# Kernel tuning notes

Hardware: AMD Instinct MI355X
Metric: run time of the kernel (lower is better)

Reference implementation:

```python
import jax, jax.numpy as jnp
import numpy as np

B, N, E = 64, 128, 512
F_NODE, F_EDGE = 16, 8
NODE_SIZE = EDGE_SIZE = 64
NUM_STEPS, N_ITER, OMEGA = 3, 8, 0.75
CUTOFF, SMEAR, EPS = 50.0, -0.39, 1e-6


def mila(x):
    # mila with beta=-1: x * tanh(softplus(x - 1))
    return x * jnp.tanh(jax.nn.softplus(x - 1.0))


def ssp(x):
    return jax.nn.softplus(x) + 1e-3


def setup_inputs():
    key = jax.random.key(0)
    ks = iter(jax.random.split(key, 64))
    def nrm(shape, s=1.0):
        return jax.random.normal(next(ks), shape, jnp.float32) * s
    def he(shape):
        return nrm(shape, (2.0 / shape[-2]) ** 0.5)
    inp = {}
    inp['nodes1'] = nrm((N, F_NODE))
    inp['edges1'] = nrm((E, F_EDGE))
    inp['senders1'] = jax.random.randint(next(ks), (E,), 0, N)
    inp['receivers1'] = jax.random.randint(next(ks), (E,), 0, N)
    inp['nodes2'] = nrm((N, F_NODE))
    inp['edges2'] = nrm((E, F_EDGE))
    inp['senders2'] = jax.random.randint(next(ks), (E,), 0, N)
    inp['receivers2'] = jax.random.randint(next(ks), (E,), 0, N)
    c1 = jax.random.uniform(next(ks), (B, N, 3), jnp.float32, 0.0, 10.0)
    c2 = jax.random.uniform(next(ks), (B, N, 3), jnp.float32, 0.0, 10.0) + jnp.array([12.0, 0.0, 0.0])
    inp['coords1'], inp['coords2'] = c1, c2
    inp['distance_matrices'] = jnp.linalg.norm(c1[:, :, None, :] - c2[:, None, :, :], axis=-1)
    inp['multipoles'] = nrm((2, B, N, 1), 0.2)
    inp['W_emb_node'], inp['b_emb_node'] = he((F_NODE, NODE_SIZE)), jnp.zeros((NODE_SIZE,))
    inp['W_emb_edge'], inp['b_emb_edge'] = he((F_EDGE, EDGE_SIZE)), jnp.zeros((EDGE_SIZE,))
    inp['W_gn_edge'] = he((NUM_STEPS, EDGE_SIZE + 2 * NODE_SIZE, EDGE_SIZE))
    inp['b_gn_edge'] = jnp.zeros((NUM_STEPS, EDGE_SIZE))
    inp['W_gn_node'] = he((NUM_STEPS, NODE_SIZE + EDGE_SIZE, NODE_SIZE))
    inp['b_gn_node'] = jnp.zeros((NUM_STEPS, NODE_SIZE))
    inp['pp_W0'], inp['pp_b0'] = he((2 * NODE_SIZE, NODE_SIZE)), jnp.zeros((NODE_SIZE,))
    inp['pp_W1'], inp['pp_b1'] = he((NODE_SIZE, NODE_SIZE)), jnp.zeros((NODE_SIZE,))
    inp['pp_W2'], inp['pp_b2'] = he((NODE_SIZE, 5)), jnp.zeros((5,))
    inp['ap_W0'], inp['ap_b0'] = he((NODE_SIZE, NODE_SIZE)), jnp.zeros((NODE_SIZE,))
    inp['ap_W1'], inp['ap_b1'] = he((NODE_SIZE, NODE_SIZE)), jnp.zeros((NODE_SIZE,))
    inp['ap_W2'], inp['ap_b2'] = he((NODE_SIZE, 5)), jnp.zeros((5,))
    return inp


def _gnn(nodes, edges, senders, receivers, Wen, ben, Wee, bee, Wge, bge, Wgn, bgn):
    # GraphIndependent embedding, then NUM_STEPS InteractionNetwork blocks
    n = mila(nodes @ Wen + ben)
    e = mila(edges @ Wee + bee)
    for s in range(NUM_STEPS):
        e_in = jnp.concatenate([e, n[receivers], n[senders]], axis=-1)
        e = mila(e_in @ Wge[s] + bge[s])
        agg = jax.ops.segment_sum(e, receivers, num_segments=N)
        n = mila(jnp.concatenate([n, agg], axis=-1) @ Wgn[s] + bgn[s])
    return n


def _mlp3(x, W0, b0, W1, b1, W2, b2):
    h = mila(x @ W0 + b0)
    h = mila(h @ W1 + b1)
    return ssp(h @ W2 + b2)


def _induction(coords1, coords2, pol1, pol2, dist, q1, q2):
    # Thole-damped SCF induced dipoles between the two monomers
    r12 = coords1[:, :, None, :] - coords2[:, None, :, :]            # [B,N,N,3]
    R = dist[..., None]                                              # [B,N,N,1]
    R3 = R ** 3 + EPS
    au = jnp.sqrt(pol1[:, 0][:, None] * pol2[:, 0][None, :]) + EPS   # [N,N]
    u3 = dist ** 3 / au                                              # [B,N,N]
    exu = jnp.exp(SMEAR * u3)
    lam3 = (1.0 - exu)[..., None]
    lam5 = (1.0 - (1.0 - SMEAR * u3) * exu)[..., None]
    E0_1 = jnp.sum(q2[:, None, :, None] * lam3 * r12 / R3, axis=2)   # [B,N,3]
    E0_2 = jnp.sum(q1[:, :, None, None] * lam3 * (-r12) / R3, axis=1)
    eye = jnp.eye(3, dtype=coords1.dtype)
    T12 = (3.0 * lam5[..., None] * r12[..., :, None] * r12[..., None, :] / (R ** 5 + EPS)[..., None]
           - lam3[..., None] * eye / R3[..., None])                  # [B,N,N,3,3]
    p1, p2 = pol1[None], pol2[None]                                  # [1,N,1]
    mu1, mu2 = p1 * E0_1, p2 * E0_2
    def step(carry, _):
        m1, m2 = carry
        f1 = E0_1 + jnp.einsum('bijkl,bjl->bik', T12, m2)
        f2 = E0_2 + jnp.einsum('bijkl,bil->bjk', T12, m1)
        m1n = (1.0 - OMEGA) * m1 + OMEGA * p1 * f1
        m2n = (1.0 - OMEGA) * m2 + OMEGA * p2 * f2
        return (m1n, m2n), None
    (mu1, mu2), _ = jax.lax.scan(step, (mu1, mu2), None, length=N_ITER)
    energy = -0.5 * (jnp.sum(mu1 * E0_1, axis=(1, 2)) + jnp.sum(mu2 * E0_2, axis=(1, 2)))
    return energy, mu1, mu2


def _forward(nodes1, edges1, senders1, receivers1, nodes2, edges2, senders2, receivers2,
             coords1, coords2, multipoles, distance_matrices,
             W_emb_node, b_emb_node, W_emb_edge, b_emb_edge,
             W_gn_edge, b_gn_edge, W_gn_node, b_gn_node,
             pp_W0, pp_b0, pp_W1, pp_b1, pp_W2, pp_b2,
             ap_W0, ap_b0, ap_W1, ap_b1, ap_W2, ap_b2):
    Bsz = distance_matrices.shape[0]
    h1 = jnp.argmax(nodes1, axis=-1) == 0
    h2 = jnp.argmax(nodes2, axis=-1) == 0
    i1 = jnp.repeat(jnp.arange(N), N)
    i2 = jnp.tile(jnp.arange(N), N)
    R1 = distance_matrices.reshape(Bsz, -1, 1)                       # [B,P,1]
    R2 = R1 ** 2
    Rx1 = coords2[:, i2] - coords1[:, i1]                            # [B,P,3]
    # GNN embeddings (shared weights for both monomers)
    feats1 = _gnn(nodes1, edges1, senders1, receivers1, W_emb_node, b_emb_node,
                  W_emb_edge, b_emb_edge, W_gn_edge, b_gn_edge, W_gn_node, b_gn_node)
    feats2 = _gnn(nodes2, edges2, senders2, receivers2, W_emb_node, b_emb_node,
                  W_emb_edge, b_emb_edge, W_gn_edge, b_gn_edge, W_gn_node, b_gn_node)
    f1p, f2p = feats1[i1], feats2[i2]                                # [P,64]
    params = (_mlp3(jnp.concatenate([f1p, f2p], -1), pp_W0, pp_b0, pp_W1, pp_b1, pp_W2, pp_b2)
              + _mlp3(jnp.concatenate([f2p, f1p], -1), pp_W0, pp_b0, pp_W1, pp_b1, pp_W2, pp_b2))
    ap1 = _mlp3(feats1, ap_W0, ap_b0, ap_W1, ap_b1, ap_W2, ap_b2)    # [N,5]
    ap2 = _mlp3(feats2, ap_W0, ap_b0, ap_W1, ap_b1, ap_W2, ap_b2)
    a_d1, pol1, K1, dq1, a_e1 = jnp.split(ap1, 5, axis=-1)
    a_d2, pol2, K2, dq2, a_e2 = jnp.split(ap2, 5, axis=-1)
    q1, q2 = multipoles[0], multipoles[1]                            # [B,N,1]
    qe1 = jnp.where(h1[None, :, None], 1.0 - q1, 2.0 + dq1[None] - q1)
    qe2 = jnp.where(h2[None, :, None], 1.0 - q2, 2.0 + dq2[None] - q2)
    Rs = R1 + EPS
    B0 = 1.0 / Rs
    # induction (SCF) + charge transfer
    in_term, mu1, mu2 = _induction(coords1, coords2, pol1, pol2, distance_matrices,
                                   q1[..., 0], q2[..., 0])
    A_ct, b_ct = params[:, 3:4], params[:, 4:5]
    in_term = in_term - jnp.sum(A_ct[None] * jnp.exp(-b_ct[None] * R1), axis=(-1, -2))
    # BJ dispersion
    C6, C8, C10 = params[:, 0:1], params[:, 1:2], params[:, 2:3]
    r0_2 = C8 / (C6 + EPS)
    R6, R8, R10 = R2 ** 3, R2 ** 4, R2 ** 5
    bj = -(C6 / (R6 + r0_2 ** 3) + C8 / (R8 + r0_2 ** 4) + C10 / (R10 + r0_2 ** 5))
    disp_term = jnp.sum(jnp.where(R2 < CUTOFF ** 2, bj, 0.0), axis=(-1, -2))
    # damped charge-charge electrostatics
    q1p = jnp.take(q1, i1, axis=1)
    q2p = jnp.take(q2, i2, axis=1)
    bd = jnp.sqrt(a_d1[i1] * a_d2[i2])[None]                         # [1,P,1]
    fdamp = 1.0 - (1.0 + 0.5 * bd * R1) * jnp.exp(-bd * R1)
    es_term = jnp.sum(q1p * q2p * fdamp * B0, axis=(-1, -2))
    # anisotropic exchange (induced-dipole anisotropy along the pair axis)
    rhat = Rx1 * B0
    m1p = jnp.take(mu1, i1, axis=1)
    m2p = jnp.take(mu2, i2, axis=1)
    proj = jnp.sum((m1p - m2p) * rhat, axis=-1, keepdims=True)
    be = jnp.sqrt(a_e1[i1] * a_e2[i2])[None]
    Kp = (K1[i1] * K2[i2])[None]
    qe1p = jnp.take(qe1, i1, axis=1)
    qe2p = jnp.take(qe2, i2, axis=1)
    ex_term = jnp.sum(Kp * qe1p * qe2p * (1.0 + proj) * jnp.exp(-be * R1) * B0, axis=(-1, -2))
    total = ex_term + disp_term + es_term + in_term
    return total, es_term, in_term, ex_term, disp_term


def reference(nodes1, edges1, senders1, receivers1, nodes2, edges2, senders2, receivers2,
              coords1, coords2, multipoles, distance_matrices,
              W_emb_node, b_emb_node, W_emb_edge, b_emb_edge,
              W_gn_edge, b_gn_edge, W_gn_node, b_gn_node,
              pp_W0, pp_b0, pp_W1, pp_b1, pp_W2, pp_b2,
              ap_W0, ap_b0, ap_W1, ap_b1, ap_W2, ap_b2):
    return _forward(nodes1, edges1, senders1, receivers1, nodes2, edges2, senders2, receivers2,
                    coords1, coords2, multipoles, distance_matrices,
                    W_emb_node, b_emb_node, W_emb_edge, b_emb_edge,
                    W_gn_edge, b_gn_edge, W_gn_node, b_gn_node,
                    pp_W0, pp_b0, pp_W1, pp_b1, pp_W2, pp_b2,
                    ap_W0, ap_b0, ap_W1, ap_b1, ap_W2, ap_b2)
```

## Files before the change

kernel.cpp:

```cpp
#include <hip/hip_runtime.h>

#define DEVI __device__ __forceinline__

DEVI float b2f(unsigned short u){
  union { unsigned u; float f; } v; v.u = ((unsigned)u) << 16; return v.f;
}
DEVI unsigned short f2b(float f){
  union { float f; unsigned u; } v; v.f = f;
  unsigned r = (v.u + 0x7fffu + ((v.u >> 16) & 1u)) >> 16;
  return (unsigned short)r;
}
DEVI float splus(float x){ return fmaxf(x, 0.f) + log1pf(expf(-fabsf(x))); }
DEVI float mila(float x){ return x * tanhf(splus(x - 1.f)); }
DEVI float ssp_(float x){ return splus(x) + 0.001f; }

constexpr int OFF_N   = 0;
constexpr int OFF_E   = 16384;
constexpr int OFF_A1  = 81920;
constexpr int OFF_A2  = 90112;
constexpr int OFF_B1  = 98304;
constexpr int OFF_B2  = 106496;
constexpr int OFF_APT = 114688;
constexpr int OFF_HM  = 115968;
constexpr int OFF_PAR = 116224;
constexpr int OFF_MU1 = 198144;
constexpr int OFF_MU2 = 230912;
constexpr int OFF_ACC = 263680;
constexpr int OFF_FLAG= 263936;
constexpr int OFF_MIR = 264192;
constexpr int MTOT    = 1211280;
constexpr int OFF_C35 = 1475472;
constexpr int OFF_E01 = 3572624;
constexpr int OFF_E02 = 3605392;
constexpr int OFF_MUB = 3638160;
constexpr int OFF_CNT = 3703696;
constexpr int OFF_LST = 3703952;
constexpr size_t WS_NEED_NEW = (size_t)(3720336) * 4;

#define M_NODES1 (mir + 0)
#define M_EDGES1 (mir + 2048)
#define M_NODES2 (mir + 6144)
#define M_EDGES2 (mir + 8192)
#define M_C1     (mir + 12288)
#define M_C2     (mir + 36864)
#define M_DIST   (mir + 61440)
#define M_MP     (mir + 1110016)
#define M_WEN    (mir + 1126400)
#define M_BEN    (mir + 1127424)
#define M_WEE    (mir + 1127488)
#define M_BEE    (mir + 1128000)
#define M_WGE    (mir + 1128064)
#define M_BGE    (mir + 1164928)
#define M_WGN    (mir + 1165120)
#define M_BGN    (mir + 1189696)
#define M_PPW0   (mir + 1189888)
#define M_PPB0   (mir + 1198080)
#define M_PPW1   (mir + 1198144)
#define M_PPB1   (mir + 1202240)
#define M_PPW2   (mir + 1202304)
#define M_PPB2   (mir + 1202624)
#define M_APW0   (mir + 1202632)
#define M_APB0   (mir + 1206728)
#define M_APW1   (mir + 1206792)
#define M_APB1   (mir + 1210888)
#define M_APW2   (mir + 1210952)
#define M_APB2   (mir + 1211272)

__constant__ int c_moff[29] = {0,2048,6144,8192,12288,36864,61440,1110016,
  1126400,1127424,1127488,1128000,1128064,1164928,1165120,1189696,1189888,
  1198080,1198144,1202240,1202304,1202624,1202632,1206728,1206792,1210888,
  1210952,1211272,1211280};
__constant__ int c_mcnt[28] = {2048,4096,2048,4096,24576,24576,1048576,16384,
  1024,64,512,64,36864,192,24576,192,8192,64,4096,64,320,5,4096,64,4096,64,320,5};

__global__ void k_probe(const unsigned short* dist_u, float* ws)
{
  int t = threadIdx.x;
  float v = b2f(dist_u[t]);
  bool ok = (v > 0.25f) && (v < 512.f);
  unsigned long long m = __ballot(ok);
  if (t == 0) ws[OFF_FLAG] = (m == ~0ull) ? 1.f : 0.f;
}

__global__ void __launch_bounds__(512) k_build(const int* recv1, const int* recv2, float* ws)
{
  __shared__ int cnt[128];
  int g = blockIdx.x, t = threadIdx.x;
  if (t < 128) cnt[t] = 0;
  __syncthreads();
  const int* recv = g ? recv2 : recv1;
  int nd = recv[t];
  int pos = atomicAdd(&cnt[nd], 1);
  if (pos < 64) ((int*)ws)[OFF_LST + (g*128+nd)*64 + pos] = t;
  __syncthreads();
  if (t < 128) ((int*)ws)[OFF_CNT + g*128 + t] = cnt[t];
}

__global__ void __launch_bounds__(256) k_convert(
    const void* s0, const void* s1, const void* s2, const void* s3,
    const void* s4, const void* s5, const void* s6, const void* s7,
    const void* s8, const void* s9, const void* s10, const void* s11,
    const void* s12, const void* s13, const void* s14, const void* s15,
    const void* s16, const void* s17, const void* s18, const void* s19,
    const void* s20, const void* s21, const void* s22, const void* s23,
    const void* s24, const void* s25, const void* s26, const void* s27,
    float* ws)
{
  const void* sp[28] = {s0,s1,s2,s3,s4,s5,s6,s7,s8,s9,s10,s11,s12,s13,
                        s14,s15,s16,s17,s18,s19,s20,s21,s22,s23,s24,s25,s26,s27};
  int g = blockIdx.x * 256 + threadIdx.x;
  if (g >= MTOT) return;
  bool isbf = ws[OFF_FLAG] != 0.f;
  int lo = 0, hi = 28;
  #pragma unroll
  for (int st = 0; st < 5; st++) {
    int mid = (lo + hi) >> 1;
    if (g >= c_moff[mid]) lo = mid; else hi = mid;
  }
  int local = g - c_moff[lo];
  if (local < c_mcnt[lo]) {
    float v = isbf ? b2f(((const unsigned short*)sp[lo])[local])
                   : ((const float*)sp[lo])[local];
    ws[OFF_MIR + g] = v;
  }
}

__global__ void __launch_bounds__(256) k_emb(float* ws)
{
  const float* mir = ws + OFF_MIR;
  int t = threadIdx.x, c = t & 63;
  int row = blockIdx.x * 4 + (t >> 6);
  if (row < 256) {
    int g = row >> 7, nd = row & 127;
    const float* src = g ? M_NODES2 : M_NODES1;
    const float* W = M_WEN; const float* bb = M_BEN;
    float acc = bb[c];
    for (int k = 0; k < 16; k++) acc += src[nd*16+k] * W[k*64+c];
    ws[OFF_N + (g*128+nd)*64 + c] = mila(acc);
  } else {
    int er = row - 256; int g = er >> 9, ed = er & 511;
    const float* src = g ? M_EDGES2 : M_EDGES1;
    const float* W = M_WEE; const float* bb = M_BEE;
    float acc = bb[c];
    for (int k = 0; k < 8; k++) acc += src[ed*8+k] * W[k*64+c];
    ws[OFF_E + (g*512+ed)*64 + c] = mila(acc);
  }
}

__global__ void __launch_bounds__(256) k_edge(const int* recv1, const int* send1,
    const int* recv2, const int* send2, int s, float* ws)
{
  const float* mir = ws + OFF_MIR;
  __shared__ float ein[4][192];
  int t = threadIdx.x;
  int le = t >> 6, c = t & 63;
  int eidx = blockIdx.x * 4;
  const float* n = ws + OFF_N;
  const float* e = ws + OFF_E;
  for (int q = t; q < 768; q += 256) {
    int ee = q / 192, k = q % 192;
    int ge = eidx + ee; int g = ge >> 9, ed = ge & 511;
    const int* recv = g ? recv2 : recv1;
    const int* send = g ? send2 : send1;
    float v;
    if (k < 64)       v = e[(g*512+ed)*64 + k];
    else if (k < 128) v = n[(g*128+recv[ed])*64 + (k-64)];
    else              v = n[(g*128+send[ed])*64 + (k-128)];
    ein[ee][k] = v;
  }
  __syncthreads();
  const float* W = M_WGE + s*192*64;
  float acc = M_BGE[s*64+c];
  for (int k = 0; k < 192; k++) acc += ein[le][k] * W[k*64+c];
  int ge = eidx + le; int g = ge >> 9, ed = ge & 511;
  ws[OFF_E + (g*512+ed)*64 + c] = mila(acc);
}

__global__ void __launch_bounds__(64) k_node(const int* recv1, const int* recv2,
    int s, float* ws)
{
  const float* mir = ws + OFF_MIR;
  __shared__ float xin[128];
  int c = threadIdx.x;
  int g = blockIdx.x >> 7, nd = blockIdx.x & 127;
  const float* n = ws + OFF_N;
  const float* e = ws + OFF_E;
  int cnt = ((const int*)ws)[OFF_CNT + g*128 + nd];
  float agg = 0.f;
  if (cnt <= 64) {
    const int* lst = (const int*)ws + OFF_LST + (g*128+nd)*64;
    for (int q = 0; q < cnt; q++) {
      int ed = lst[q];
      agg += e[(g*512+ed)*64 + c];
    }
  } else {
    const int* recv = g ? recv2 : recv1;
    for (int ed = 0; ed < 512; ed++)
      if (recv[ed] == nd) agg += e[(g*512+ed)*64 + c];
  }
  xin[c] = n[(g*128+nd)*64 + c];
  xin[64 + c] = agg;
  __syncthreads();
  const float* W = M_WGN + s*128*64;
  float acc = M_BGN[s*64+c];
  for (int k = 0; k < 128; k++) acc += xin[k] * W[k*64+c];
  ws[OFF_N + (g*128+nd)*64 + c] = mila(acc);
}

__global__ void __launch_bounds__(256) k_prep(float* ws)
{
  const float* mir = ws + OFF_MIR;
  __shared__ float sh[4][64], sh2[4][64];
  int t = threadIdx.x;
  const float* n = ws + OFF_N;
  if (blockIdx.x < 128) {
    int T = blockIdx.x >> 5, rg = blockIdx.x & 31;
    int r = rg*4 + (t >> 6), c = t & 63;
    const float* f = (T == 0 || T == 2) ? n : (n + 128*64);
    int wofs = (T == 0 || T == 3) ? 0 : 64;
    const float* W0 = M_PPW0;
    float acc = (T == 1 || T == 2) ? M_PPB0[c] : 0.f;
    for (int k = 0; k < 64; k++) acc += f[r*64+k] * W0[(wofs+k)*64 + c];
    if (T == 0)      ws[OFF_A1 + r*64 + c] = acc;
    else if (T == 1) ws[OFF_A2 + c*128 + r] = acc;
    else if (T == 2) ws[OFF_B1 + r*64 + c] = acc;
    else             ws[OFF_B2 + c*128 + r] = acc;
  } else {
    int b2i = blockIdx.x - 128;
    int g = b2i >> 5, grp = b2i & 31;
    int ln = t >> 6, c = t & 63;
    int nd = grp*4 + ln;
    const float* f = n + (g*128+nd)*64;
    float acc = M_APB0[c];
    for (int k = 0; k < 64; k++) acc += f[k] * M_APW0[k*64+c];
    sh[ln][c] = mila(acc);
    __syncthreads();
    acc = M_APB1[c];
    for (int k = 0; k < 64; k++) acc += sh[ln][k] * M_APW1[k*64+c];
    sh2[ln][c] = mila(acc);
    __syncthreads();
    if (c < 5) {
      float a2 = M_APB2[c];
      for (int k = 0; k < 64; k++) a2 += sh2[ln][k] * M_APW2[k*5+c];
      ws[OFF_APT + (g*5+c)*128 + nd] = ssp_(a2);
    }
    if (c == 0) {
      const float* ns = (g ? M_NODES2 : M_NODES1) + nd*16;
      float v0 = ns[0];
      float ok = 1.f;
      for (int k = 1; k < 16; k++) if (ns[k] > v0) ok = 0.f;
      ws[OFF_HM + g*128 + nd] = ok;
    }
  }
}

__global__ void __launch_bounds__(256) k_pair(float* ws)
{
  const float* mir = ws + OFF_MIR;
  float* params = ws + OFF_PAR;
  __shared__ float W1s[4096];
  __shared__ float W2s[320];
  __shared__ float b1s[64], b2s[8], bases[64];
  __shared__ float h0s[4096];
  __shared__ float opart[64][4][5];
  int t = threadIdx.x;
  int jl = t & 63, h = t >> 6;
  int i = blockIdx.x >> 2, dir = (blockIdx.x >> 1) & 1, jh = blockIdx.x & 1;
  const float* base = ws + (dir ? OFF_B1 : OFF_A1) + i*64;
  const float* oT   = ws + (dir ? OFF_B2 : OFF_A2) + jh*64;
  #pragma unroll
  for (int q = 0; q < 16; q++) W1s[q*256 + t] = M_PPW1[q*256 + t];
  for (int q = t; q < 320; q += 256) W2s[q] = M_PPW2[q];
  if (t < 64) { b1s[t] = M_PPB1[t]; bases[t] = base[t]; }
  if (t >= 64 && t < 72) b2s[t-64] = (t-64 < 5) ? M_PPB2[t-64] : 0.f;
  __syncthreads();
  #pragma unroll
  for (int q = 0; q < 16; q++) {
    int idx = q*256 + t;
    int c = idx >> 6, j2 = idx & 63;
    h0s[idx] = mila(bases[c] + oT[c*128 + j2]);
  }
  __syncthreads();
  float h1c[16];
  #pragma unroll
  for (int k = 0; k < 16; k++) h1c[k] = b1s[h*16 + k];
  for (int c = 0; c < 64; c++) {
    float h0c = h0s[c*64 + jl];
    const float4* w4 = (const float4*)&W1s[c*64 + h*16];
    float4 wa = w4[0], wb = w4[1], wc = w4[2], wd = w4[3];
    h1c[0]  += h0c*wa.x; h1c[1]  += h0c*wa.y; h1c[2]  += h0c*wa.z; h1c[3]  += h0c*wa.w;
    h1c[4]  += h0c*wb.x; h1c[5]  += h0c*wb.y; h1c[6]  += h0c*wb.z; h1c[7]  += h0c*wb.w;
    h1c[8]  += h0c*wc.x; h1c[9]  += h0c*wc.y; h1c[10] += h0c*wc.z; h1c[11] += h0c*wc.w;
    h1c[12] += h0c*wd.x; h1c[13] += h0c*wd.y; h1c[14] += h0c*wd.z; h1c[15] += h0c*wd.w;
  }
  float o5p[5] = {0.f, 0.f, 0.f, 0.f, 0.f};
  #pragma unroll
  for (int k = 0; k < 16; k++) {
    float hk = mila(h1c[k]);
    int kk = h*16 + k;
    #pragma unroll
    for (int o = 0; o < 5; o++) o5p[o] += hk * W2s[kk*5 + o];
  }
  #pragma unroll
  for (int o = 0; o < 5; o++) opart[jl][h][o] = o5p[o];
  __syncthreads();
  if (t < 64) {
    int p = i*128 + jh*64 + t;
    #pragma unroll
    for (int o = 0; o < 5; o++) {
      float val = b2s[o] + opart[t][0][o] + opart[t][1][o]
                         + opart[t][2][o] + opart[t][3][o];
      atomicAdd(&params[p*5 + o], ssp_(val));
    }
  }
}

__global__ void __launch_bounds__(1024) k_ind_all(float* ws)
{
  const float* mir = ws + OFF_MIR;
  const float* apT = ws + OFF_APT;
  __shared__ float sC3[128*132];
  __shared__ float sC5[128*132];
  __shared__ float4 c1s[128], c2s[128], m1s[128], m2s[128];
  __shared__ float4 e01s[128], e02s[128], f1s[128], f2s[128];
  __shared__ float p1s[128], p2s[128], q1s[128], q2s[128];
  __shared__ float esum[128];
  int b = blockIdx.x, t = threadIdx.x;
  if (t < 128) {
    c1s[t] = make_float4(M_C1[(b*128+t)*3], M_C1[(b*128+t)*3+1], M_C1[(b*128+t)*3+2], 0.f);
    c2s[t] = make_float4(M_C2[(b*128+t)*3], M_C2[(b*128+t)*3+1], M_C2[(b*128+t)*3+2], 0.f);
    p1s[t] = apT[128 + t];
    p2s[t] = apT[(5+1)*128 + t];
    q1s[t] = M_MP[b*128 + t];
    q2s[t] = M_MP[8192 + b*128 + t];
  }
  __syncthreads();
  int il = t >> 3, sub = t & 7;
  {
    float4 c1 = c1s[il];
    float p1 = p1s[il];
    float ex = 0, ey = 0, ez = 0;
    #pragma unroll 4
    for (int jj = 0; jj < 16; jj++) {
      int j = sub + 8*jj;
      float R = M_DIST[b*16384 + il*128 + j];
      float R2 = R*R, R3 = R2*R, R5 = R3*R2;
      float au = sqrtf(p1 * p2s[j]) + 1e-6f;
      float u3 = R3 / au;
      float exu = expf(-0.39f * u3);
      float c3 = (1.f - exu) / (R3 + 1e-6f);
      float c5 = 3.f * (1.f - (1.f + 0.39f*u3) * exu) / (R5 + 1e-6f);
      sC3[il*132 + j] = c3;
      sC5[il*132 + j] = c5;
      float w = q2s[j] * c3;
      ex += w*(c1.x - c2s[j].x); ey += w*(c1.y - c2s[j].y); ez += w*(c1.z - c2s[j].z);
    }
    #pragma unroll
    for (int m = 1; m <= 4; m <<= 1) {
      ex += __shfl_xor(ex, m, 64); ey += __shfl_xor(ey, m, 64); ez += __shfl_xor(ez, m, 64);
    }
    if (sub == 0) e01s[il] = make_float4(ex, ey, ez, 0.f);
  }
  __syncthreads();
  {
    float4 c2 = c2s[il];
    float ex = 0, ey = 0, ez = 0;
    #pragma unroll 4
    for (int jj = 0; jj < 16; jj++) {
      int i = sub + 8*jj;
      float c3 = sC3[i*132 + il];
      float w = q1s[i] * c3;
      ex -= w*(c1s[i].x - c2.x); ey -= w*(c1s[i].y - c2.y); ez -= w*(c1s[i].z - c2.z);
    }
    #pragma unroll
    for (int m = 1; m <= 4; m <<= 1) {
      ex += __shfl_xor(ex, m, 64); ey += __shfl_xor(ey, m, 64); ez += __shfl_xor(ez, m, 64);
    }
    if (sub == 0) e02s[il] = make_float4(ex, ey, ez, 0.f);
  }
  __syncthreads();
  if (t < 128) {
    float4 e1 = e01s[t], e2 = e02s[t];
    m1s[t] = make_float4(p1s[t]*e1.x, p1s[t]*e1.y, p1s[t]*e1.z, 0.f);
    m2s[t] = make_float4(p2s[t]*e2.x, p2s[t]*e2.y, p2s[t]*e2.z, 0.f);
  }
  __syncthreads();
  for (int it = 0; it < 8; it++) {
    {
      float4 c1 = c1s[il];
      float fx = 0, fy = 0, fz = 0;
      #pragma unroll 4
      for (int jj = 0; jj < 16; jj++) {
        int j = sub + 8*jj;
        float c3 = sC3[il*132 + j];
        float c5 = sC5[il*132 + j];
        float4 m2 = m2s[j], c2 = c2s[j];
        float rx = c1.x - c2.x, ry = c1.y - c2.y, rz = c1.z - c2.z;
        float dot = rx*m2.x + ry*m2.y + rz*m2.z;
        float a = c5 * dot;
        fx += a*rx - c3*m2.x; fy += a*ry - c3*m2.y; fz += a*rz - c3*m2.z;
      }
      #pragma unroll
      for (int m = 1; m <= 4; m <<= 1) {
        fx += __shfl_xor(fx, m, 64); fy += __shfl_xor(fy, m, 64); fz += __shfl_xor(fz, m, 64);
      }
      if (sub == 0) f1s[il] = make_float4(fx, fy, fz, 0.f);
    }
    {
      float4 c2 = c2s[il];
      float fx = 0, fy = 0, fz = 0;
      #pragma unroll 4
      for (int jj = 0; jj < 16; jj++) {
        int i = sub + 8*jj;
        float c3 = sC3[i*132 + il];
        float c5 = sC5[i*132 + il];
        float4 m1 = m1s[i], c1 = c1s[i];
        float rx = c1.x - c2.x, ry = c1.y - c2.y, rz = c1.z - c2.z;
        float dot = rx*m1.x + ry*m1.y + rz*m1.z;
        float a = c5 * dot;
        fx += a*rx - c3*m1.x; fy += a*ry - c3*m1.y; fz += a*rz - c3*m1.z;
      }
      #pragma unroll
      for (int m = 1; m <= 4; m <<= 1) {
        fx += __shfl_xor(fx, m, 64); fy += __shfl_xor(fy, m, 64); fz += __shfl_xor(fz, m, 64);
      }
      if (sub == 0) f2s[il] = make_float4(fx, fy, fz, 0.f);
    }
    __syncthreads();
    if (t < 128) {
      float4 f1 = f1s[t], e1 = e01s[t], mo1 = m1s[t];
      float4 f2 = f2s[t], e2 = e02s[t], mo2 = m2s[t];
      float p1 = p1s[t], p2 = p2s[t];
      m1s[t] = make_float4(0.25f*mo1.x + 0.75f*p1*(e1.x + f1.x),
                           0.25f*mo1.y + 0.75f*p1*(e1.y + f1.y),
                           0.25f*mo1.z + 0.75f*p1*(e1.z + f1.z), 0.f);
      m2s[t] = make_float4(0.25f*mo2.x + 0.75f*p2*(e2.x + f2.x),
                           0.25f*mo2.y + 0.75f*p2*(e2.y + f2.y),
                           0.25f*mo2.z + 0.75f*p2*(e2.z + f2.z), 0.f);
    }
    __syncthreads();
  }
  if (t < 128) {
    float4 m1 = m1s[t], m2 = m2s[t], e1 = e01s[t], e2 = e02s[t];
    esum[t] = m1.x*e1.x + m1.y*e1.y + m1.z*e1.z
            + m2.x*e2.x + m2.y*e2.y + m2.z*e2.z;
    *(float4*)&ws[OFF_MU1 + (b*128+t)*4] = m1;
    *(float4*)&ws[OFF_MU2 + (b*128+t)*4] = m2;
  }
  __syncthreads();
  if (t == 0) {
    float s = 0.f;
    for (int k = 0; k < 128; k++) s += esum[k];
    ws[OFF_ACC + 64 + b] = -0.5f * s;
  }
}

__global__ void __launch_bounds__(512) k_induction(float* ws)
{
  const float* mir = ws + OFF_MIR;
  __shared__ __align__(16) float sC3[128*132];
  __shared__ __align__(16) float sC5[128*132];
  __shared__ __align__(16) float sC1[128][4], sC2[128][4];
  __shared__ __align__(16) float sE01[128][4], sE02[128][4];
  __shared__ __align__(16) float sM1[128][4], sM2[128][4];
  __shared__ __align__(16) float sF1[128][4], sF2[128][4];
  __shared__ float sQ1[128], sQ2[128], sP1[128], sP2[128];
  __shared__ float sred[8];
  int b = blockIdx.x, t = threadIdx.x;
  const float* apT = ws + OFF_APT;
  if (t < 128) {
    for (int k = 0; k < 3; k++) {
      sC1[t][k] = M_C1[(b*128+t)*3 + k];
      sC2[t][k] = M_C2[(b*128+t)*3 + k];
    }
    sC1[t][3] = 0.f; sC2[t][3] = 0.f;
    sQ1[t] = M_MP[b*128 + t];
    sQ2[t] = M_MP[8192 + b*128 + t];
    sP1[t] = apT[(0*5+1)*128 + t];
    sP2[t] = apT[(1*5+1)*128 + t];
    for (int k = 0; k < 4; k++) { sE01[t][k] = 0.f; sE02[t][k] = 0.f; }
  }
  __syncthreads();
  int x = t & 127, quad = t >> 7;
  float c1x = sC1[x][0], c1y = sC1[x][1], c1z = sC1[x][2];
  float c2x = sC2[x][0], c2y = sC2[x][1], c2z = sC2[x][2];
  float p2j = sP2[x];
  float e2x = 0, e2y = 0, e2z = 0;
  for (int s = 0; s < 32; s++) {
    int i = quad*32 + s;
    float R = M_DIST[b*16384 + i*128 + x];
    float rx = sC1[i][0] - c2x, ry = sC1[i][1] - c2y, rz = sC1[i][2] - c2z;
    float R2 = R*R, R3 = R2*R, R5 = R3*R2;
    float au = sqrtf(sP1[i] * p2j) + 1e-6f;
    float u3 = R3 / au;
    float exu = expf(-0.39f * u3);
    float lam3 = 1.f - exu;
    float lam5 = 1.f - (1.f + 0.39f*u3) * exu;
    float c3 = lam3 / (R3 + 1e-6f);
    float c5 = 3.f * lam5 / (R5 + 1e-6f);
    sC3[i*132 + x] = c3;
    sC5[i*132 + x] = c5;
    float w = sQ1[i] * c3;
    e2x -= w*rx; e2y -= w*ry; e2z -= w*rz;
  }
  atomicAdd(&sE02[x][0], e2x); atomicAdd(&sE02[x][1], e2y); atomicAdd(&sE02[x][2], e2z);
  __syncthreads();
  float e1x = 0, e1y = 0, e1z = 0;
  for (int s = 0; s < 8; s++) {
    int j0 = quad*32 + s*4;
    float4 c3q = *(const float4*)&sC3[x*132 + j0];
    #pragma unroll
    for (int jj = 0; jj < 4; jj++) {
      int j = j0 + jj;
      float c3v = ((const float*)&c3q)[jj];
      float rx = c1x - sC2[j][0], ry = c1y - sC2[j][1], rz = c1z - sC2[j][2];
      float w = sQ2[j] * c3v;
      e1x += w*rx; e1y += w*ry; e1z += w*rz;
    }
  }
  atomicAdd(&sE01[x][0], e1x); atomicAdd(&sE01[x][1], e1y); atomicAdd(&sE01[x][2], e1z);
  __syncthreads();
  if (t < 128) {
    for (int k = 0; k < 4; k++) {
      sM1[t][k] = sP1[t] * sE01[t][k];
      sM2[t][k] = sP2[t] * sE02[t][k];
      sF1[t][k] = 0.f; sF2[t][k] = 0.f;
    }
  }
  __syncthreads();
  for (int it = 0; it < 8; it++) {
    float f1x = 0, f1y = 0, f1z = 0;
    for (int s = 0; s < 8; s++) {
      int j0 = quad*32 + s*4;
      float4 c3q = *(const float4*)&sC3[x*132 + j0];
      float4 c5q = *(const float4*)&sC5[x*132 + j0];
      #pragma unroll
      for (int jj = 0; jj < 4; jj++) {
        int j = j0 + jj;
        float4 m2 = *(const float4*)&sM2[j][0];
        float rx = c1x - sC2[j][0], ry = c1y - sC2[j][1], rz = c1z - sC2[j][2];
        float dot = rx*m2.x + ry*m2.y + rz*m2.z;
        float a = ((const float*)&c5q)[jj] * dot;
        float c3v = ((const float*)&c3q)[jj];
        f1x += a*rx - c3v*m2.x;
        f1y += a*ry - c3v*m2.y;
        f1z += a*rz - c3v*m2.z;
      }
    }
    atomicAdd(&sF1[x][0], f1x); atomicAdd(&sF1[x][1], f1y); atomicAdd(&sF1[x][2], f1z);
    float f2x = 0, f2y = 0, f2z = 0;
    for (int s = 0; s < 32; s++) {
      int i = quad*32 + s;
      float c3v = sC3[i*132 + x], c5v = sC5[i*132 + x];
      float4 m1 = *(const float4*)&sM1[i][0];
      float rx = sC1[i][0] - c2x, ry = sC1[i][1] - c2y, rz = sC1[i][2] - c2z;
      float dot = rx*m1.x + ry*m1.y + rz*m1.z;
      float a = c5v * dot;
      f2x += a*rx - c3v*m1.x;
      f2y += a*ry - c3v*m1.y;
      f2z += a*rz - c3v*m1.z;
    }
    atomicAdd(&sF2[x][0], f2x); atomicAdd(&sF2[x][1], f2y); atomicAdd(&sF2[x][2], f2z);
    __syncthreads();
    if (t < 128) {
      for (int k = 0; k < 3; k++) {
        float f1 = sE01[t][k] + sF1[t][k];
        float f2 = sE02[t][k] + sF2[t][k];
        sM1[t][k] = 0.25f*sM1[t][k] + 0.75f*sP1[t]*f1;
        sM2[t][k] = 0.25f*sM2[t][k] + 0.75f*sP2[t]*f2;
        sF1[t][k] = 0.f; sF2[t][k] = 0.f;
      }
    }
    __syncthreads();
  }
  float part = 0.f;
  if (t < 128) {
    for (int k = 0; k < 3; k++) part += sM1[t][k]*sE01[t][k] + sM2[t][k]*sE02[t][k];
    *(float4*)&ws[OFF_MU1 + (b*128+t)*4] = *(float4*)&sM1[t][0];
    *(float4*)&ws[OFF_MU2 + (b*128+t)*4] = *(float4*)&sM2[t][0];
  }
  for (int m = 32; m >= 1; m >>= 1) part += __shfl_xor(part, m, 64);
  if ((t & 63) == 0) sred[t >> 6] = part;
  __syncthreads();
  if (t == 0) {
    float s = 0.f;
    for (int w = 0; w < 8; w++) s += sred[w];
    ws[OFF_ACC + 64 + b] = -0.5f * s;
  }
}

__global__ void __launch_bounds__(256) k_terms(float* ws)
{
  const float* mir = ws + OFF_MIR;
  int b = blockIdx.x >> 2, q = blockIdx.x & 3;
  int t = threadIdx.x;
  const float* par = ws + OFF_PAR;
  const float* apT = ws + OFF_APT;
  const float* hm  = ws + OFF_HM;
  const float* mu1 = ws + OFF_MU1;
  const float* mu2 = ws + OFF_MU2;
  float es = 0, ct = 0, ex = 0, dp = 0;
  for (int s = 0; s < 16; s++) {
    int p = q*4096 + s*256 + t;
    int i = p >> 7, j = p & 127;
    float C6 = par[p*5+0], C8 = par[p*5+1], C10 = par[p*5+2];
    float Act = par[p*5+3], bct = par[p*5+4];
    float R = M_DIST[b*16384 + p];
    float Rs = R + 1e-6f;
    float B0 = 1.f / Rs;
    float R2 = R*R;
    float R6 = R2*R2*R2, R8 = R6*R2, R10 = R8*R2;
    float r0 = C8 / (C6 + 1e-6f);
    float D6 = r0*r0*r0, D8 = D6*r0, D10 = D8*r0;
    if (R2 < 2500.f) dp -= C6/(R6+D6) + C8/(R8+D8) + C10/(R10+D10);
    ct += Act * expf(-bct * R);
    float q1v = M_MP[b*128 + i];
    float q2v = M_MP[8192 + b*128 + j];
    float ad1 = apT[0*128 + i],   ad2 = apT[(5+0)*128 + j];
    float k1v = apT[2*128 + i],   k2v = apT[(5+2)*128 + j];
    float ae1 = apT[4*128 + i],   ae2 = apT[(5+4)*128 + j];
    float dq1 = apT[3*128 + i],   dq2 = apT[(5+3)*128 + j];
    float bd = sqrtf(ad1*ad2), be = sqrtf(ae1*ae2), Kp = k1v*k2v;
    float ebd = expf(-bd * R);
    float fd = 1.f - (1.f + 0.5f*bd*R) * ebd;
    es += q1v * q2v * fd * B0;
    float rxx = M_C2[(b*128+j)*3+0] - M_C1[(b*128+i)*3+0];
    float rxy = M_C2[(b*128+j)*3+1] - M_C1[(b*128+i)*3+1];
    float rxz = M_C2[(b*128+j)*3+2] - M_C1[(b*128+i)*3+2];
    float m1x = mu1[(b*128+i)*4+0], m1y = mu1[(b*128+i)*4+1], m1z = mu1[(b*128+i)*4+2];
    float m2x = mu2[(b*128+j)*4+0], m2y = mu2[(b*128+j)*4+1], m2z = mu2[(b*128+j)*4+2];
    float proj = ((m1x-m2x)*rxx + (m1y-m2y)*rxy + (m1z-m2z)*rxz) * B0;
    float h1v = hm[i], h2v = hm[128 + j];
    float qe1 = h1v > 0.5f ? (1.f - q1v) : (2.f + dq1 - q1v);
    float qe2 = h2v > 0.5f ? (1.f - q2v) : (2.f + dq2 - q2v);
    ex += Kp * qe1 * qe2 * (1.f + proj) * expf(-be * R) * B0;
  }
  __shared__ float sred[4][4];
  for (int m = 32; m >= 1; m >>= 1) {
    es += __shfl_xor(es, m, 64); ct += __shfl_xor(ct, m, 64);
    ex += __shfl_xor(ex, m, 64); dp += __shfl_xor(dp, m, 64);
  }
  int w = t >> 6;
  if ((t & 63) == 0) { sred[w][0] = es; sred[w][1] = ct; sred[w][2] = ex; sred[w][3] = dp; }
  __syncthreads();
  if (t == 0) {
    float a0 = 0, a1 = 0, a2 = 0, a3 = 0;
    for (int ww = 0; ww < 4; ww++) { a0 += sred[ww][0]; a1 += sred[ww][1]; a2 += sred[ww][2]; a3 += sred[ww][3]; }
    atomicAdd(&ws[OFF_ACC +   0 + b], a0);
    atomicAdd(&ws[OFF_ACC +  64 + b], -a1);
    atomicAdd(&ws[OFF_ACC + 128 + b], a2);
    atomicAdd(&ws[OFF_ACC + 192 + b], a3);
  }
}

__global__ void __launch_bounds__(64) k_total(const float* ws, void* outv)
{
  int b = threadIdx.x;
  float es  = ws[OFF_ACC +   0 + b];
  float inv = ws[OFF_ACC +  64 + b];
  float ex  = ws[OFF_ACC + 128 + b];
  float dp  = ws[OFF_ACC + 192 + b];
  float tot = ex + dp + es + inv;
  if (ws[OFF_FLAG] != 0.f) {
    unsigned short* out = (unsigned short*)outv;
    out[b]       = f2b(tot);
    out[64 + b]  = f2b(es);
    out[128 + b] = f2b(inv);
    out[192 + b] = f2b(ex);
    out[256 + b] = f2b(dp);
  } else {
    float* out = (float*)outv;
    out[b]       = tot;
    out[64 + b]  = es;
    out[128 + b] = inv;
    out[192 + b] = ex;
    out[256 + b] = dp;
  }
}

extern "C" void kernel_launch(void* const* d_in, const int* in_sizes, int n_in,
                              void* d_out, int out_size, void* d_ws, size_t ws_size,
                              hipStream_t stream)
{
  const int* send1 = (const int*)d_in[2];
  const int* recv1 = (const int*)d_in[3];
  const int* send2 = (const int*)d_in[6];
  const int* recv2 = (const int*)d_in[7];
  float* ws = (float*)d_ws;

  hipMemsetAsync((void*)(ws + OFF_PAR), 0, 16384*5*sizeof(float), stream);
  hipMemsetAsync((void*)(ws + OFF_ACC), 0, 256*sizeof(float), stream);

  k_probe<<<1, 64, 0, stream>>>((const unsigned short*)d_in[10], ws);
  k_build<<<2, 512, 0, stream>>>(recv1, recv2, ws);
  k_convert<<<(MTOT + 255) / 256, 256, 0, stream>>>(
      d_in[0], d_in[1], d_in[4], d_in[5], d_in[8], d_in[9], d_in[10], d_in[11],
      d_in[12], d_in[13], d_in[14], d_in[15], d_in[16], d_in[17], d_in[18], d_in[19],
      d_in[20], d_in[21], d_in[22], d_in[23], d_in[24], d_in[25], d_in[26], d_in[27],
      d_in[28], d_in[29], d_in[30], d_in[31], ws);

  k_emb<<<320, 256, 0, stream>>>(ws);
  for (int s = 0; s < 3; s++) {
    k_edge<<<256, 256, 0, stream>>>(recv1, send1, recv2, send2, s, ws);
    k_node<<<256, 64, 0, stream>>>(recv1, recv2, s, ws);
  }
  k_prep<<<192, 256, 0, stream>>>(ws);
  k_pair<<<512, 256, 0, stream>>>(ws);

  if (ws_size >= WS_NEED_NEW) {
    k_ind_all<<<64, 1024, 0, stream>>>(ws);
  } else {
    k_induction<<<64, 512, 0, stream>>>(ws);
  }

  k_terms<<<256, 256, 0, stream>>>(ws);
  k_total<<<1, 64, 0, stream>>>(ws, d_out);
}
```

Before: 349.1 us.

## Merge setup kernels into one launch and read distances directly from input

Folds the dtype probe, receiver list build and both workspace memsets into a single k_convert launch. The distance matrix is no longer mirrored into the workspace; k_ind_all and k_terms read it from the raw input with a per-element bf16/fp32 branch. The C3/C5 shared arrays become one interleaved float2 array, and the fallback induction kernel is removed. The aim is fewer launches and less copy traffic, at the cost of every block redundantly running the probe and losing the small-workspace fallback path.

Result: faster. 294.2 us (-15.7%).

```diff
diff --git a/kernel.cpp b/kernel.cpp
--- a/kernel.cpp
+++ b/kernel.cpp
@@ -13,6 +13,9 @@
 DEVI float splus(float x){ return fmaxf(x, 0.f) + log1pf(expf(-fabsf(x))); }
 DEVI float mila(float x){ return x * tanhf(splus(x - 1.f)); }
 DEVI float ssp_(float x){ return splus(x) + 0.001f; }
+DEVI float rdist(const void* p, long idx, bool isbf){
+  return isbf ? b2f(((const unsigned short*)p)[idx]) : ((const float*)p)[idx];
+}
 
 constexpr int OFF_N   = 0;
 constexpr int OFF_E   = 16384;
@@ -28,14 +31,9 @@
 constexpr int OFF_ACC = 263680;
 constexpr int OFF_FLAG= 263936;
 constexpr int OFF_MIR = 264192;
-constexpr int MTOT    = 1211280;
-constexpr int OFF_C35 = 1475472;
-constexpr int OFF_E01 = 3572624;
-constexpr int OFF_E02 = 3605392;
-constexpr int OFF_MUB = 3638160;
+constexpr int MTOT    = 162698;
 constexpr int OFF_CNT = 3703696;
 constexpr int OFF_LST = 3703952;
-constexpr size_t WS_NEED_NEW = (size_t)(3720336) * 4;
 
 #define M_NODES1 (mir + 0)
 #define M_EDGES1 (mir + 2048)
@@ -43,58 +41,33 @@
 #define M_EDGES2 (mir + 8192)
 #define M_C1     (mir + 12288)
 #define M_C2     (mir + 36864)
-#define M_DIST   (mir + 61440)
-#define M_MP     (mir + 1110016)
-#define M_WEN    (mir + 1126400)
-#define M_BEN    (mir + 1127424)
-#define M_WEE    (mir + 1127488)
-#define M_BEE    (mir + 1128000)
-#define M_WGE    (mir + 1128064)
-#define M_BGE    (mir + 1164928)
-#define M_WGN    (mir + 1165120)
-#define M_BGN    (mir + 1189696)
-#define M_PPW0   (mir + 1189888)
-#define M_PPB0   (mir + 1198080)
-#define M_PPW1   (mir + 1198144)
-#define M_PPB1   (mir + 1202240)
-#define M_PPW2   (mir + 1202304)
-#define M_PPB2   (mir + 1202624)
-#define M_APW0   (mir + 1202632)
-#define M_APB0   (mir + 1206728)
-#define M_APW1   (mir + 1206792)
-#define M_APB1   (mir + 1210888)
-#define M_APW2   (mir + 1210952)
-#define M_APB2   (mir + 1211272)
-
-__constant__ int c_moff[29] = {0,2048,6144,8192,12288,36864,61440,1110016,
-  1126400,1127424,1127488,1128000,1128064,1164928,1165120,1189696,1189888,
-  1198080,1198144,1202240,1202304,1202624,1202632,1206728,1206792,1210888,
-  1210952,1211272,1211280};
-__constant__ int c_mcnt[28] = {2048,4096,2048,4096,24576,24576,1048576,16384,
+#define M_MP     (mir + 61440)
+#define M_WEN    (mir + 77824)
+#define M_BEN    (mir + 78848)
+#define M_WEE    (mir + 78912)
+#define M_BEE    (mir + 79424)
+#define M_WGE    (mir + 79488)
+#define M_BGE    (mir + 116352)
+#define M_WGN    (mir + 116544)
+#define M_BGN    (mir + 141120)
+#define M_PPW0   (mir + 141312)
+#define M_PPB0   (mir + 149504)
+#define M_PPW1   (mir + 149568)
+#define M_PPB1   (mir + 153664)
+#define M_PPW2   (mir + 153728)
+#define M_PPB2   (mir + 154048)
+#define M_APW0   (mir + 154053)
+#define M_APB0   (mir + 158149)
+#define M_APW1   (mir + 158213)
+#define M_APB1   (mir + 162309)
+#define M_APW2   (mir + 162373)
+#define M_APB2   (mir + 162693)
+
+__constant__ int c_moff[28] = {0,2048,6144,8192,12288,36864,61440,77824,
+  78848,78912,79424,79488,116352,116544,141120,141312,149504,149568,
+  153664,153728,154048,154053,158149,158213,162309,162373,162693,162698};
+__constant__ int c_mcnt[27] = {2048,4096,2048,4096,24576,24576,16384,
   1024,64,512,64,36864,192,24576,192,8192,64,4096,64,320,5,4096,64,4096,64,320,5};
-
-__global__ void k_probe(const unsigned short* dist_u, float* ws)
-{
-  int t = threadIdx.x;
-  float v = b2f(dist_u[t]);
-  bool ok = (v > 0.25f) && (v < 512.f);
-  unsigned long long m = __ballot(ok);
-  if (t == 0) ws[OFF_FLAG] = (m == ~0ull) ? 1.f : 0.f;
-}
-
-__global__ void __launch_bounds__(512) k_build(const int* recv1, const int* recv2, float* ws)
-{
-  __shared__ int cnt[128];
-  int g = blockIdx.x, t = threadIdx.x;
-  if (t < 128) cnt[t] = 0;
-  __syncthreads();
-  const int* recv = g ? recv2 : recv1;
-  int nd = recv[t];
-  int pos = atomicAdd(&cnt[nd], 1);
-  if (pos < 64) ((int*)ws)[OFF_LST + (g*128+nd)*64 + pos] = t;
-  __syncthreads();
-  if (t < 128) ((int*)ws)[OFF_CNT + g*128 + t] = cnt[t];
-}
 
 __global__ void __launch_bounds__(256) k_convert(
     const void* s0, const void* s1, const void* s2, const void* s3,
@@ -103,25 +76,55 @@
     const void* s12, const void* s13, const void* s14, const void* s15,
     const void* s16, const void* s17, const void* s18, const void* s19,
     const void* s20, const void* s21, const void* s22, const void* s23,
-    const void* s24, const void* s25, const void* s26, const void* s27,
-    float* ws)
-{
-  const void* sp[28] = {s0,s1,s2,s3,s4,s5,s6,s7,s8,s9,s10,s11,s12,s13,
-                        s14,s15,s16,s17,s18,s19,s20,s21,s22,s23,s24,s25,s26,s27};
-  int g = blockIdx.x * 256 + threadIdx.x;
-  if (g >= MTOT) return;
-  bool isbf = ws[OFF_FLAG] != 0.f;
-  int lo = 0, hi = 28;
-  #pragma unroll
-  for (int st = 0; st < 5; st++) {
-    int mid = (lo + hi) >> 1;
-    if (g >= c_moff[mid]) lo = mid; else hi = mid;
-  }
-  int local = g - c_moff[lo];
-  if (local < c_mcnt[lo]) {
-    float v = isbf ? b2f(((const unsigned short*)sp[lo])[local])
-                   : ((const float*)sp[lo])[local];
-    ws[OFF_MIR + g] = v;
+    const void* s24, const void* s25, const void* s26,
+    const void* distraw, const int* recv1, const int* recv2, float* ws)
+{
+  __shared__ int sflag;
+  __shared__ int bcnt[128];
+  int t = threadIdx.x, bid = blockIdx.x;
+  if (t < 64) {
+    float v = b2f(((const unsigned short*)distraw)[t]);
+    bool ok = (v > 0.25f) && (v < 512.f);
+    unsigned long long m = __ballot(ok);
+    if (t == 0) sflag = (m == ~0ull) ? 1 : 0;
+  }
+  __syncthreads();
+  bool isbf = sflag != 0;
+  if (bid < 636) {
+    const void* sp[27] = {s0,s1,s2,s3,s4,s5,s6,s7,s8,s9,s10,s11,s12,s13,
+                          s14,s15,s16,s17,s18,s19,s20,s21,s22,s23,s24,s25,s26};
+    int g = bid*256 + t;
+    if (g >= MTOT) return;
+    int lo = 0, hi = 27;
+    #pragma unroll
+    for (int st = 0; st < 5; st++) {
+      int mid = (lo + hi) >> 1;
+      if (g >= c_moff[mid]) lo = mid; else hi = mid;
+    }
+    int local = g - c_moff[lo];
+    if (local < c_mcnt[lo]) {
+      float v = isbf ? b2f(((const unsigned short*)sp[lo])[local])
+                     : ((const float*)sp[lo])[local];
+      ws[OFF_MIR + g] = v;
+    }
+  } else if (bid < 956) {
+    ws[OFF_PAR + (bid-636)*256 + t] = 0.f;
+  } else if (bid == 956) {
+    ws[OFF_ACC + t] = 0.f;
+    if (t == 0) ws[OFF_FLAG] = isbf ? 1.f : 0.f;
+  } else {
+    int g = bid - 957;
+    const int* recv = g ? recv2 : recv1;
+    if (t < 128) bcnt[t] = 0;
+    __syncthreads();
+    for (int pass = 0; pass < 2; pass++) {
+      int ed = pass*256 + t;
+      int nd = recv[ed];
+      int pos = atomicAdd(&bcnt[nd], 1);
+      if (pos < 64) ((int*)ws)[OFF_LST + (g*128+nd)*64 + pos] = ed;
+    }
+    __syncthreads();
+    if (t < 128) ((int*)ws)[OFF_CNT + g*128 + t] = bcnt[t];
   }
 }
 
@@ -133,16 +136,14 @@
   if (row < 256) {
     int g = row >> 7, nd = row & 127;
     const float* src = g ? M_NODES2 : M_NODES1;
-    const float* W = M_WEN; const float* bb = M_BEN;
-    float acc = bb[c];
-    for (int k = 0; k < 16; k++) acc += src[nd*16+k] * W[k*64+c];
+    float acc = M_BEN[c];
+    for (int k = 0; k < 16; k++) acc += src[nd*16+k] * M_WEN[k*64+c];
     ws[OFF_N + (g*128+nd)*64 + c] = mila(acc);
   } else {
     int er = row - 256; int g = er >> 9, ed = er & 511;
     const float* src = g ? M_EDGES2 : M_EDGES1;
-    const float* W = M_WEE; const float* bb = M_BEE;
-    float acc = bb[c];
-    for (int k = 0; k < 8; k++) acc += src[ed*8+k] * W[k*64+c];
+    float acc = M_BEE[c];
+    for (int k = 0; k < 8; k++) acc += src[ed*8+k] * M_WEE[k*64+c];
     ws[OFF_E + (g*512+ed)*64 + c] = mila(acc);
   }
 }
@@ -218,9 +219,8 @@
     int r = rg*4 + (t >> 6), c = t & 63;
     const float* f = (T == 0 || T == 2) ? n : (n + 128*64);
     int wofs = (T == 0 || T == 3) ? 0 : 64;
-    const float* W0 = M_PPW0;
     float acc = (T == 1 || T == 2) ? M_PPB0[c] : 0.f;
-    for (int k = 0; k < 64; k++) acc += f[r*64+k] * W0[(wofs+k)*64 + c];
+    for (int k = 0; k < 64; k++) acc += f[r*64+k] * M_PPW0[(wofs+k)*64 + c];
     if (T == 0)      ws[OFF_A1 + r*64 + c] = acc;
     else if (T == 1) ws[OFF_A2 + c*128 + r] = acc;
     else if (T == 2) ws[OFF_B1 + r*64 + c] = acc;
@@ -315,17 +315,17 @@
   }
 }
 
-__global__ void __launch_bounds__(1024) k_ind_all(float* ws)
+__global__ void __launch_bounds__(1024) k_ind_all(const void* distp, float* ws)
 {
   const float* mir = ws + OFF_MIR;
   const float* apT = ws + OFF_APT;
-  __shared__ float sC3[128*132];
-  __shared__ float sC5[128*132];
+  __shared__ __align__(8) float2 sC35[128*132];
   __shared__ float4 c1s[128], c2s[128], m1s[128], m2s[128];
   __shared__ float4 e01s[128], e02s[128], f1s[128], f2s[128];
   __shared__ float p1s[128], p2s[128], q1s[128], q2s[128];
   __shared__ float esum[128];
   int b = blockIdx.x, t = threadIdx.x;
+  bool isbf = ws[OFF_FLAG] != 0.f;
   if (t < 128) {
     c1s[t] = make_float4(M_C1[(b*128+t)*3], M_C1[(b*128+t)*3+1], M_C1[(b*128+t)*3+2], 0.f);
     c2s[t] = make_float4(M_C2[(b*128+t)*3], M_C2[(b*128+t)*3+1], M_C2[(b*128+t)*3+2], 0.f);
@@ -343,15 +343,14 @@
     #pragma unroll 4
     for (int jj = 0; jj < 16; jj++) {
       int j = sub + 8*jj;
-      float R = M_DIST[b*16384 + il*128 + j];
+      float R = rdist(distp, (long)b*16384 + il*128 + j, isbf);
       float R2 = R*R, R3 = R2*R, R5 = R3*R2;
       float au = sqrtf(p1 * p2s[j]) + 1e-6f;
       float u3 = R3 / au;
       float exu = expf(-0.39f * u3);
       float c3 = (1.f - exu) / (R3 + 1e-6f);
       float c5 = 3.f * (1.f - (1.f + 0.39f*u3) * exu) / (R5 + 1e-6f);
-      sC3[il*132 + j] = c3;
-      sC5[il*132 + j] = c5;
+      sC35[il*132 + j] = make_float2(c3, c5);
       float w = q2s[j] * c3;
       ex += w*(c1.x - c2s[j].x); ey += w*(c1.y - c2s[j].y); ez += w*(c1.z - c2s[j].z);
     }
@@ -368,7 +367,7 @@
     #pragma unroll 4
     for (int jj = 0; jj < 16; jj++) {
       int i = sub + 8*jj;
-      float c3 = sC3[i*132 + il];
+      float c3 = sC35[i*132 + il].x;
       float w = q1s[i] * c3;
       ex -= w*(c1s[i].x - c2.x); ey -= w*(c1s[i].y - c2.y); ez -= w*(c1s[i].z - c2.z);
     }
@@ -392,13 +391,12 @@
       #pragma unroll 4
       for (int jj = 0; jj < 16; jj++) {
         int j = sub + 8*jj;
-        float c3 = sC3[il*132 + j];
-        float c5 = sC5[il*132 + j];
+        float2 cc = sC35[il*132 + j];
         float4 m2 = m2s[j], c2 = c2s[j];
         float rx = c1.x - c2.x, ry = c1.y - c2.y, rz = c1.z - c2.z;
         float dot = rx*m2.x + ry*m2.y + rz*m2.z;
-        float a = c5 * dot;
-        fx += a*rx - c3*m2.x; fy += a*ry - c3*m2.y; fz += a*rz - c3*m2.z;
+        float a = cc.y * dot;
+        fx += a*rx - cc.x*m2.x; fy += a*ry - cc.x*m2.y; fz += a*rz - cc.x*m2.z;
       }
       #pragma unroll
       for (int m = 1; m <= 4; m <<= 1) {
@@ -412,13 +410,12 @@
       #pragma unroll 4
       for (int jj = 0; jj < 16; jj++) {
         int i = sub + 8*jj;
-        float c3 = sC3[i*132 + il];
-        float c5 = sC5[i*132 + il];
+        float2 cc = sC35[i*132 + il];
         float4 m1 = m1s[i], c1 = c1s[i];
         float rx = c1.x - c2.x, ry = c1.y - c2.y, rz = c1.z - c2.z;
         float dot = rx*m1.x + ry*m1.y + rz*m1.z;
-        float a = c5 * dot;
-        fx += a*rx - c3*m1.x; fy += a*ry - c3*m1.y; fz += a*rz - c3*m1.z;
+        float a = cc.y * dot;
+        fx += a*rx - cc.x*m1.x; fy += a*ry - cc.x*m1.y; fz += a*rz - cc.x*m1.z;
       }
       #pragma unroll
       for (int m = 1; m <= 4; m <<= 1) {
@@ -455,145 +452,12 @@
   }
 }
 
-__global__ void __launch_bounds__(512) k_induction(float* ws)
-{
-  const float* mir = ws + OFF_MIR;
-  __shared__ __align__(16) float sC3[128*132];
-  __shared__ __align__(16) float sC5[128*132];
-  __shared__ __align__(16) float sC1[128][4], sC2[128][4];
-  __shared__ __align__(16) float sE01[128][4], sE02[128][4];
-  __shared__ __align__(16) float sM1[128][4], sM2[128][4];
-  __shared__ __align__(16) float sF1[128][4], sF2[128][4];
-  __shared__ float sQ1[128], sQ2[128], sP1[128], sP2[128];
-  __shared__ float sred[8];
-  int b = blockIdx.x, t = threadIdx.x;
-  const float* apT = ws + OFF_APT;
-  if (t < 128) {
-    for (int k = 0; k < 3; k++) {
-      sC1[t][k] = M_C1[(b*128+t)*3 + k];
-      sC2[t][k] = M_C2[(b*128+t)*3 + k];
-    }
-    sC1[t][3] = 0.f; sC2[t][3] = 0.f;
-    sQ1[t] = M_MP[b*128 + t];
-    sQ2[t] = M_MP[8192 + b*128 + t];
-    sP1[t] = apT[(0*5+1)*128 + t];
-    sP2[t] = apT[(1*5+1)*128 + t];
-    for (int k = 0; k < 4; k++) { sE01[t][k] = 0.f; sE02[t][k] = 0.f; }
-  }
-  __syncthreads();
-  int x = t & 127, quad = t >> 7;
-  float c1x = sC1[x][0], c1y = sC1[x][1], c1z = sC1[x][2];
-  float c2x = sC2[x][0], c2y = sC2[x][1], c2z = sC2[x][2];
-  float p2j = sP2[x];
-  float e2x = 0, e2y = 0, e2z = 0;
-  for (int s = 0; s < 32; s++) {
-    int i = quad*32 + s;
-    float R = M_DIST[b*16384 + i*128 + x];
-    float rx = sC1[i][0] - c2x, ry = sC1[i][1] - c2y, rz = sC1[i][2] - c2z;
-    float R2 = R*R, R3 = R2*R, R5 = R3*R2;
-    float au = sqrtf(sP1[i] * p2j) + 1e-6f;
-    float u3 = R3 / au;
-    float exu = expf(-0.39f * u3);
-    float lam3 = 1.f - exu;
-    float lam5 = 1.f - (1.f + 0.39f*u3) * exu;
-    float c3 = lam3 / (R3 + 1e-6f);
-    float c5 = 3.f * lam5 / (R5 + 1e-6f);
-    sC3[i*132 + x] = c3;
-    sC5[i*132 + x] = c5;
-    float w = sQ1[i] * c3;
-    e2x -= w*rx; e2y -= w*ry; e2z -= w*rz;
-  }
-  atomicAdd(&sE02[x][0], e2x); atomicAdd(&sE02[x][1], e2y); atomicAdd(&sE02[x][2], e2z);
-  __syncthreads();
-  float e1x = 0, e1y = 0, e1z = 0;
-  for (int s = 0; s < 8; s++) {
-    int j0 = quad*32 + s*4;
-    float4 c3q = *(const float4*)&sC3[x*132 + j0];
-    #pragma unroll
-    for (int jj = 0; jj < 4; jj++) {
-      int j = j0 + jj;
-      float c3v = ((const float*)&c3q)[jj];
-      float rx = c1x - sC2[j][0], ry = c1y - sC2[j][1], rz = c1z - sC2[j][2];
-      float w = sQ2[j] * c3v;
-      e1x += w*rx; e1y += w*ry; e1z += w*rz;
-    }
-  }
-  atomicAdd(&sE01[x][0], e1x); atomicAdd(&sE01[x][1], e1y); atomicAdd(&sE01[x][2], e1z);
-  __syncthreads();
-  if (t < 128) {
-    for (int k = 0; k < 4; k++) {
-      sM1[t][k] = sP1[t] * sE01[t][k];
-      sM2[t][k] = sP2[t] * sE02[t][k];
-      sF1[t][k] = 0.f; sF2[t][k] = 0.f;
-    }
-  }
-  __syncthreads();
-  for (int it = 0; it < 8; it++) {
-    float f1x = 0, f1y = 0, f1z = 0;
-    for (int s = 0; s < 8; s++) {
-      int j0 = quad*32 + s*4;
-      float4 c3q = *(const float4*)&sC3[x*132 + j0];
-      float4 c5q = *(const float4*)&sC5[x*132 + j0];
-      #pragma unroll
-      for (int jj = 0; jj < 4; jj++) {
-        int j = j0 + jj;
-        float4 m2 = *(const float4*)&sM2[j][0];
-        float rx = c1x - sC2[j][0], ry = c1y - sC2[j][1], rz = c1z - sC2[j][2];
-        float dot = rx*m2.x + ry*m2.y + rz*m2.z;
-        float a = ((const float*)&c5q)[jj] * dot;
-        float c3v = ((const float*)&c3q)[jj];
-        f1x += a*rx - c3v*m2.x;
-        f1y += a*ry - c3v*m2.y;
-        f1z += a*rz - c3v*m2.z;
-      }
-    }
-    atomicAdd(&sF1[x][0], f1x); atomicAdd(&sF1[x][1], f1y); atomicAdd(&sF1[x][2], f1z);
-    float f2x = 0, f2y = 0, f2z = 0;
-    for (int s = 0; s < 32; s++) {
-      int i = quad*32 + s;
-      float c3v = sC3[i*132 + x], c5v = sC5[i*132 + x];
-      float4 m1 = *(const float4*)&sM1[i][0];
-      float rx = sC1[i][0] - c2x, ry = sC1[i][1] - c2y, rz = sC1[i][2] - c2z;
-      float dot = rx*m1.x + ry*m1.y + rz*m1.z;
-      float a = c5v * dot;
-      f2x += a*rx - c3v*m1.x;
-      f2y += a*ry - c3v*m1.y;
-      f2z += a*rz - c3v*m1.z;
-    }
-    atomicAdd(&sF2[x][0], f2x); atomicAdd(&sF2[x][1], f2y); atomicAdd(&sF2[x][2], f2z);
-    __syncthreads();
-    if (t < 128) {
-      for (int k = 0; k < 3; k++) {
-        float f1 = sE01[t][k] + sF1[t][k];
-        float f2 = sE02[t][k] + sF2[t][k];
-        sM1[t][k] = 0.25f*sM1[t][k] + 0.75f*sP1[t]*f1;
-        sM2[t][k] = 0.25f*sM2[t][k] + 0.75f*sP2[t]*f2;
-        sF1[t][k] = 0.f; sF2[t][k] = 0.f;
-      }
-    }
-    __syncthreads();
-  }
-  float part = 0.f;
-  if (t < 128) {
-    for (int k = 0; k < 3; k++) part += sM1[t][k]*sE01[t][k] + sM2[t][k]*sE02[t][k];
-    *(float4*)&ws[OFF_MU1 + (b*128+t)*4] = *(float4*)&sM1[t][0];
-    *(float4*)&ws[OFF_MU2 + (b*128+t)*4] = *(float4*)&sM2[t][0];
-  }
-  for (int m = 32; m >= 1; m >>= 1) part += __shfl_xor(part, m, 64);
-  if ((t & 63) == 0) sred[t >> 6] = part;
-  __syncthreads();
-  if (t == 0) {
-    float s = 0.f;
-    for (int w = 0; w < 8; w++) s += sred[w];
-    ws[OFF_ACC + 64 + b] = -0.5f * s;
-  }
-}
-
-__global__ void __launch_bounds__(256) k_terms(float* ws)
+__global__ void __launch_bounds__(256) k_terms(const void* distp, float* ws)
 {
   const float* mir = ws + OFF_MIR;
   int b = blockIdx.x >> 2, q = blockIdx.x & 3;
   int t = threadIdx.x;
+  bool isbf = ws[OFF_FLAG] != 0.f;
   const float* par = ws + OFF_PAR;
   const float* apT = ws + OFF_APT;
   const float* hm  = ws + OFF_HM;
@@ -605,7 +469,7 @@
     int i = p >> 7, j = p & 127;
     float C6 = par[p*5+0], C8 = par[p*5+1], C10 = par[p*5+2];
     float Act = par[p*5+3], bct = par[p*5+4];
-    float R = M_DIST[b*16384 + p];
+    float R = rdist(distp, (long)b*16384 + p, isbf);
     float Rs = R + 1e-6f;
     float B0 = 1.f / Rs;
     float R2 = R*R;
@@ -688,16 +552,12 @@
   const int* recv2 = (const int*)d_in[7];
   float* ws = (float*)d_ws;
 
-  hipMemsetAsync((void*)(ws + OFF_PAR), 0, 16384*5*sizeof(float), stream);
-  hipMemsetAsync((void*)(ws + OFF_ACC), 0, 256*sizeof(float), stream);
-
-  k_probe<<<1, 64, 0, stream>>>((const unsigned short*)d_in[10], ws);
-  k_build<<<2, 512, 0, stream>>>(recv1, recv2, ws);
-  k_convert<<<(MTOT + 255) / 256, 256, 0, stream>>>(
-      d_in[0], d_in[1], d_in[4], d_in[5], d_in[8], d_in[9], d_in[10], d_in[11],
-      d_in[12], d_in[13], d_in[14], d_in[15], d_in[16], d_in[17], d_in[18], d_in[19],
-      d_in[20], d_in[21], d_in[22], d_in[23], d_in[24], d_in[25], d_in[26], d_in[27],
-      d_in[28], d_in[29], d_in[30], d_in[31], ws);
+  k_convert<<<959, 256, 0, stream>>>(
+      d_in[0], d_in[1], d_in[4], d_in[5], d_in[8], d_in[9], d_in[11],
+      d_in[12], d_in[13], d_in[14], d_in[15], d_in[16], d_in[17], d_in[18],
+      d_in[19], d_in[20], d_in[21], d_in[22], d_in[23], d_in[24], d_in[25],
+      d_in[26], d_in[27], d_in[28], d_in[29], d_in[30], d_in[31],
+      d_in[10], recv1, recv2, ws);
 
   k_emb<<<320, 256, 0, stream>>>(ws);
   for (int s = 0; s < 3; s++) {
@@ -706,13 +566,7 @@
   }
   k_prep<<<192, 256, 0, stream>>>(ws);
   k_pair<<<512, 256, 0, stream>>>(ws);
-
-  if (ws_size >= WS_NEED_NEW) {
-    k_ind_all<<<64, 1024, 0, stream>>>(ws);
-  } else {
-    k_induction<<<64, 512, 0, stream>>>(ws);
-  }
-
-  k_terms<<<256, 256, 0, stream>>>(ws);
+  k_ind_all<<<64, 1024, 0, stream>>>(d_in[10], ws);
+  k_terms<<<256, 256, 0, stream>>>(d_in[10], ws);
   k_total<<<1, 64, 0, stream>>>(ws, d_out);
 }
```
